# Kernel tuning notes

Hardware: AMD Instinct MI355X
Metric: run time of the kernel (lower is better)

## Reference

```python
import jax, jax.numpy as jnp
import numpy as np

NUM_HEADS = 16
NUM_KV_HEADS = 8
HEAD_DIM = 128
SCALE = 1.0 / np.sqrt(HEAD_DIM)  # 0.08838834764831845
SEQ_LENS = [1536, 512, 1024, 1024]  # ragged packed sequences, total T=4096


def setup_inputs() -> dict:
    key = jax.random.key(0)
    k1, k2, k3 = jax.random.split(key, 3)
    T = sum(SEQ_LENS)
    q = jax.random.normal(k1, (T, NUM_HEADS * HEAD_DIM), dtype=jnp.float32)
    k = jax.random.normal(k2, (T, NUM_KV_HEADS * HEAD_DIM), dtype=jnp.float32)
    v = jax.random.normal(k3, (T, NUM_KV_HEADS * HEAD_DIM), dtype=jnp.float32)
    # positions restart at 0 for each packed sequence; jumps mark boundaries
    positions = jnp.asarray(np.concatenate([np.arange(L) for L in SEQ_LENS]), dtype=jnp.int32)
    return {"q": q, "k": k, "v": v, "positions": positions}


def reference(q, k, v, positions):
    T = q.shape[0]
    G = NUM_HEADS // NUM_KV_HEADS  # GQA group size
    qh = q.reshape(T, NUM_KV_HEADS, G, HEAD_DIM)
    kh = k.reshape(T, NUM_KV_HEADS, HEAD_DIM)
    vh = v.reshape(T, NUM_KV_HEADS, HEAD_DIM)
    # segment ids from position jumps (positions[i] != positions[i-1] + 1)
    jump = jnp.concatenate([
        jnp.zeros((1,), jnp.int32),
        (positions[1:] != positions[:-1] + 1).astype(jnp.int32),
    ])
    seg = jnp.cumsum(jump)  # [T]
    idx = jnp.arange(T)
    # attend only within the same packed sequence, causally
    mask = (seg[:, None] == seg[None, :]) & (idx[:, None] >= idx[None, :])  # [T, T]
    # scores: [kv_head, group, T_q, T_k]
    scores = jnp.einsum('tkgd,skd->kgts', qh, kh) * jnp.float32(SCALE)
    scores = jnp.where(mask[None, None], scores, jnp.float32(-1e30))
    p = jax.nn.softmax(scores, axis=-1)
    o = jnp.einsum('kgts,skd->tkgd', p, vh)
    return o.reshape(T, NUM_HEADS * HEAD_DIM)
```

## Files before the change

kernel.cpp:

```cpp
#include <hip/hip_runtime.h>
#include <cstdint>
#include <cstddef>

#define NUM_KV   8
#define GQA      2
#define HD       128
#define QSTRIDE  2048
#define KSTRIDE  1024
#define SCALE_LOG2E 0.12751741032075463f

typedef float    f32x4  __attribute__((ext_vector_type(4)));
typedef float    f32x2  __attribute__((ext_vector_type(2)));
typedef float    f32x16 __attribute__((ext_vector_type(16)));
typedef unsigned u32x4  __attribute__((ext_vector_type(4)));
typedef __bf16   bf16x8 __attribute__((ext_vector_type(8)));
typedef __bf16   bf16x2 __attribute__((ext_vector_type(2)));

union U8 { unsigned short u[8]; unsigned d[4]; u32x4 q; bf16x8 v; };

__device__ __forceinline__ unsigned short f2b(float f) {
    union { float f; unsigned u; } x;
    x.f = f;
    unsigned r = x.u + 0x7fffu + ((x.u >> 16) & 1u);
    return (unsigned short)(r >> 16);
}
__device__ __forceinline__ unsigned pkb(float x, float y) {
    f32x2 f = {x, y};
    bf16x2 b = __builtin_convertvector(f, bf16x2);
    union { bf16x2 b; unsigned u; } c; c.b = b;
    return c.u;
}

#define PS_STRIDE 40

__global__ __launch_bounds__(512)
void swizzle_k(const float* __restrict__ kg, unsigned short* __restrict__ Kswz,
               int T, int NT)
{
    const int tt = blockIdx.x, h = blockIdx.y;
    const int tid = threadIdx.x;
    const int c = tid >> 6, lane = tid & 63;
    const int col = lane & 31, hk = lane >> 5;
    const int row = min(tt * 32 + col, T - 1);
    const float* src = kg + (size_t)row * KSTRIDE + h * HD + c * 16 + hk * 8;
    f32x4 a = ((const f32x4*)src)[0];
    f32x4 b = ((const f32x4*)src)[1];
    u32x4 W;
    W[0] = pkb(a[0], a[1]); W[1] = pkb(a[2], a[3]);
    W[2] = pkb(b[0], b[1]); W[3] = pkb(b[2], b[3]);
    *(u32x4*)(Kswz + (((size_t)h * NT + tt) * 8 + c) * 512 + lane * 8) = W;
}

__global__ __launch_bounds__(512)
void swizzle_v(const float* __restrict__ vg, unsigned short* __restrict__ Vswz,
               int T, int NT)
{
    const int tt = blockIdx.x, h = blockIdx.y;
    const int tid = threadIdx.x;
    const int f = tid >> 6, lane = tid & 63;
    const int col = lane & 31, hk = lane >> 5;
    const int d  = (f >> 1) * 32 + col;
    const int r0 = tt * 32 + (f & 1) * 16 + hk * 8;
    float x[8];
#pragma unroll
    for (int j = 0; j < 8; ++j) {
        const int row = min(r0 + j, T - 1);
        x[j] = vg[(size_t)row * KSTRIDE + h * HD + d];
    }
    u32x4 W;
    W[0] = pkb(x[0], x[1]); W[1] = pkb(x[2], x[3]);
    W[2] = pkb(x[4], x[5]); W[3] = pkb(x[6], x[7]);
    *(u32x4*)(Vswz + (((size_t)h * NT + tt) * 8 + f) * 512 + lane * 8) = W;
}

__global__ __launch_bounds__(256, 2)
void attn_kernel(const float* __restrict__ qg, const unsigned short* __restrict__ Kswz,
                 const unsigned short* __restrict__ Vswz, const int* __restrict__ pos,
                 float* __restrict__ out, int T, int NT)
{
    __shared__ __align__(16) float Obuf[4][32 * 128];
    __shared__ float Lb[4][32];
    __shared__ __align__(16) unsigned short Ps[4][32 * PS_STRIDE];

    const int tid  = threadIdx.x;
    const int w    = tid >> 6;
    const int lane = tid & 63;
    const int col  = lane & 31;
    const int hk   = lane >> 5;

    const int bid = blockIdx.x;
    const int kvh = bid & 7;
    const int g   = (bid >> 3) & 1;
    const int qtr = bid >> 4;
    const int nq  = (T + 31) >> 5;
    const int qt  = nq - 1 - qtr;
    const int row0 = qt * 32;
    if (row0 >= T) return;
    const int hq = kvh * GQA + g;

    const int kend = min(row0 + 32, T);
    const int k_lo = row0 - pos[row0];

    const int rbase = row0 + 4 * hk;
    int rstart[16];
#pragma unroll
    for (int r = 0; r < 16; ++r) {
        const int rg = rbase + (r & 3) + 8 * (r >> 2);
        const int rc = min(rg, T - 1);
        rstart[r] = rc - pos[rc];
    }
    int rs_max = rstart[0];
#pragma unroll
    for (int r = 1; r < 16; ++r) rs_max = max(rs_max, rstart[r]);
    rs_max = max(rs_max, __shfl_xor(rs_max, 32));

    bf16x8 qf[8];
    {
        const int qr = min(row0 + col, T - 1);
        const float* qp = qg + (size_t)qr * QSTRIDE + hq * HD + hk * 8;
#pragma unroll
        for (int c = 0; c < 8; ++c) {
            f32x4 f0 = ((const f32x4*)(qp + c * 16))[0];
            f32x4 f1 = ((const f32x4*)(qp + c * 16))[1];
            U8 u;
            u.d[0] = pkb(f0[0] * SCALE_LOG2E, f0[1] * SCALE_LOG2E);
            u.d[1] = pkb(f0[2] * SCALE_LOG2E, f0[3] * SCALE_LOG2E);
            u.d[2] = pkb(f1[0] * SCALE_LOG2E, f1[1] * SCALE_LOG2E);
            u.d[3] = pkb(f1[2] * SCALE_LOG2E, f1[3] * SCALE_LOG2E);
            qf[c] = u.v;
        }
    }

    f32x16 acc[4];
#pragma unroll
    for (int nt = 0; nt < 4; ++nt)
#pragma unroll
        for (int r = 0; r < 16; ++r) acc[nt][r] = 0.f;
    float l_vec[16];
#pragma unroll
    for (int r = 0; r < 16; ++r) l_vec[r] = 0.f;

    const int t_lo = k_lo >> 5;
    const int t_hi = (kend + 31) >> 5;
    const unsigned short* kb_base = Kswz + (size_t)kvh * NT * 4096;
    const unsigned short* vb_base = Vswz + (size_t)kvh * NT * 4096;

    U8 kf[8], kfn[8], vf[8];
    int tt = t_lo + w;
    if (tt < t_hi) {
        const unsigned short* kp = kb_base + (size_t)tt * 4096 + lane * 8;
#pragma unroll
        for (int c = 0; c < 8; ++c) kf[c].q = *(const u32x4*)(kp + c * 512);
    }

    for (; tt < t_hi; tt += 4) {
        const int ttn = tt + 4;
        if (ttn < t_hi) {
            const unsigned short* kp = kb_base + (size_t)ttn * 4096 + lane * 8;
#pragma unroll
            for (int c = 0; c < 8; ++c) kfn[c].q = *(const u32x4*)(kp + c * 512);
        }
        {
            const unsigned short* vp = vb_base + (size_t)tt * 4096 + lane * 8;
#pragma unroll
            for (int f = 0; f < 8; ++f) vf[f].q = *(const u32x4*)(vp + f * 512);
        }

        f32x16 s;
#pragma unroll
        for (int r = 0; r < 16; ++r) s[r] = 0.f;
#pragma unroll
        for (int c = 0; c < 8; ++c)
            s = __builtin_amdgcn_mfma_f32_32x32x16_bf16(qf[c], kf[c].v, s, 0, 0, 0);

        const int kb  = tt * 32;
        const int key = kb + col;
        float p[16];
        if (kb >= rs_max && kb + 32 <= row0 + 1) {
#pragma unroll
            for (int r = 0; r < 16; ++r) { p[r] = exp2f(s[r]); l_vec[r] += p[r]; }
        } else {
#pragma unroll
            for (int r = 0; r < 16; ++r) {
                const int rg = rbase + (r & 3) + 8 * (r >> 2);
                const float x = (key >= rstart[r] && key <= rg) ? s[r] : -3e38f;
                p[r] = exp2f(x);
                l_vec[r] += p[r];
            }
        }

        unsigned short* Pw = (unsigned short*)Ps[w];
#pragma unroll
        for (int r = 0; r < 16; ++r)
            Pw[((r & 3) + 8 * (r >> 2) + 4 * hk) * PS_STRIDE + col] = f2b(p[r]);
        U8 pa0, pa1;
        pa0.q = *(const u32x4*)&Pw[col * PS_STRIDE + hk * 8];
        pa1.q = *(const u32x4*)&Pw[col * PS_STRIDE + 16 + hk * 8];

#pragma unroll
        for (int nt = 0; nt < 4; ++nt) {
            acc[nt] = __builtin_amdgcn_mfma_f32_32x32x16_bf16(pa0.v, vf[nt * 2].v,     acc[nt], 0, 0, 0);
            acc[nt] = __builtin_amdgcn_mfma_f32_32x32x16_bf16(pa1.v, vf[nt * 2 + 1].v, acc[nt], 0, 0, 0);
        }
#pragma unroll
        for (int c = 0; c < 8; ++c) kf[c] = kfn[c];
    }

#pragma unroll
    for (int r = 0; r < 16; ++r) {
        float sl = l_vec[r];
        sl += __shfl_xor(sl, 1);
        sl += __shfl_xor(sl, 2);
        sl += __shfl_xor(sl, 4);
        sl += __shfl_xor(sl, 8);
        sl += __shfl_xor(sl, 16);
        if (col == 0) Lb[w][(r & 3) + 8 * (r >> 2) + 4 * hk] = sl;
    }
#pragma unroll
    for (int nt = 0; nt < 4; ++nt)
#pragma unroll
        for (int r = 0; r < 16; ++r)
            Obuf[w][((r & 3) + 8 * (r >> 2) + 4 * hk) * 128 + nt * 32 + col] = acc[nt][r];

    __syncthreads();

    const int orow = tid >> 3;
    const int oc   = (tid & 7) * 16;
    const int rg   = row0 + orow;
    const float lsum = Lb[0][orow] + Lb[1][orow] + Lb[2][orow] + Lb[3][orow];
    const float inv  = (lsum > 0.f) ? (1.0f / lsum) : 0.f;
    if (rg < T) {
        float* op = out + (size_t)rg * QSTRIDE + hq * HD + oc;
#pragma unroll
        for (int j = 0; j < 4; ++j) {
            f32x4 sv = *(const f32x4*)&Obuf[0][orow * 128 + oc + j * 4];
#pragma unroll
            for (int ww = 1; ww < 4; ++ww) {
                f32x4 t = *(const f32x4*)&Obuf[ww][orow * 128 + oc + j * 4];
                sv[0] += t[0]; sv[1] += t[1]; sv[2] += t[2]; sv[3] += t[3];
            }
            sv[0] *= inv; sv[1] *= inv; sv[2] *= inv; sv[3] *= inv;
            *(f32x4*)(op + j * 4) = sv;
        }
    }
}

extern "C" void kernel_launch(void* const* d_in, const int* in_sizes, int n_in,
                              void* d_out, int out_size, void* d_ws, size_t ws_size,
                              hipStream_t stream) {
    const float* q   = (const float*)d_in[0];
    const float* k   = (const float*)d_in[1];
    const float* v   = (const float*)d_in[2];
    const int*   pos = (const int*)d_in[3];
    float* out = (float*)d_out;
    const int T  = in_sizes[0] / QSTRIDE;
    const int NT = (T + 31) / 32;

    unsigned short* Kswz = (unsigned short*)d_ws;
    unsigned short* Vswz = Kswz + (size_t)NUM_KV * NT * 4096;

    swizzle_k<<<dim3(NT, NUM_KV), 512, 0, stream>>>(k, Kswz, T, NT);
    swizzle_v<<<dim3(NT, NUM_KV), 512, 0, stream>>>(v, Vswz, T, NT);

    attn_kernel<<<dim3(NT * 16), 256, 0, stream>>>(q, Kswz, Vswz, pos, out, T, NT);
}
```

Measured before the change: 168.9 us.

## Stage K/V swizzle through LDS and prefetch V tiles one iteration ahead

The K and V swizzle kernels now load full contiguous rows with wide vector reads into shared memory and then write the MFMA-swizzled layout from LDS. This replaces the scattered per-element strided V reads. The attention loop now double-buffers V fragments alongside K, prefetching the next tile's V so its load latency overlaps the current tile's compute. This costs more registers (an extra 8 vector fragments per lane), which could lower occupancy under the launch bound of 2 blocks.

Result: slower. 213.3 us (+26.3%).

```diff
diff --git a/kernel.cpp b/kernel.cpp
--- a/kernel.cpp
+++ b/kernel.cpp
@@ -32,45 +32,80 @@
 }
 
 #define PS_STRIDE 40
-
-__global__ __launch_bounds__(512)
+#define KL_STRIDE 136
+#define VL_STRIDE 56
+
+__global__ __launch_bounds__(256)
 void swizzle_k(const float* __restrict__ kg, unsigned short* __restrict__ Kswz,
                int T, int NT)
 {
+    __shared__ __align__(16) unsigned short Ls[32 * KL_STRIDE];
     const int tt = blockIdx.x, h = blockIdx.y;
     const int tid = threadIdx.x;
-    const int c = tid >> 6, lane = tid & 63;
+
+    {
+        const int row = tid >> 3;
+        const int d0  = (tid & 7) * 16;
+        const int rg  = min(tt * 32 + row, T - 1);
+        const float* src = kg + (size_t)rg * KSTRIDE + h * HD + d0;
+        f32x4 a = ((const f32x4*)src)[0];
+        f32x4 b = ((const f32x4*)src)[1];
+        f32x4 c = ((const f32x4*)src)[2];
+        f32x4 d = ((const f32x4*)src)[3];
+        u32x4 W0, W1;
+        W0[0] = pkb(a[0], a[1]); W0[1] = pkb(a[2], a[3]);
+        W0[2] = pkb(b[0], b[1]); W0[3] = pkb(b[2], b[3]);
+        W1[0] = pkb(c[0], c[1]); W1[1] = pkb(c[2], c[3]);
+        W1[2] = pkb(d[0], d[1]); W1[3] = pkb(d[2], d[3]);
+        *(u32x4*)&Ls[row * KL_STRIDE + d0]     = W0;
+        *(u32x4*)&Ls[row * KL_STRIDE + d0 + 8] = W1;
+    }
+    __syncthreads();
+    const int f = tid >> 6, lane = tid & 63;
     const int col = lane & 31, hk = lane >> 5;
-    const int row = min(tt * 32 + col, T - 1);
-    const float* src = kg + (size_t)row * KSTRIDE + h * HD + c * 16 + hk * 8;
-    f32x4 a = ((const f32x4*)src)[0];
-    f32x4 b = ((const f32x4*)src)[1];
-    u32x4 W;
-    W[0] = pkb(a[0], a[1]); W[1] = pkb(a[2], a[3]);
-    W[2] = pkb(b[0], b[1]); W[3] = pkb(b[2], b[3]);
-    *(u32x4*)(Kswz + (((size_t)h * NT + tt) * 8 + c) * 512 + lane * 8) = W;
-}
-
-__global__ __launch_bounds__(512)
+    unsigned short* dst = Kswz + ((size_t)h * NT + tt) * 4096 + lane * 8;
+#pragma unroll
+    for (int i = 0; i < 2; ++i) {
+        const int c = f + i * 4;
+        u32x4 W = *(const u32x4*)&Ls[col * KL_STRIDE + c * 16 + hk * 8];
+        *(u32x4*)(dst + c * 512) = W;
+    }
+}
+
+__global__ __launch_bounds__(256)
 void swizzle_v(const float* __restrict__ vg, unsigned short* __restrict__ Vswz,
                int T, int NT)
 {
+    __shared__ __align__(16) unsigned short Lsv[HD * VL_STRIDE];
     const int tt = blockIdx.x, h = blockIdx.y;
     const int tid = threadIdx.x;
+
+    {
+        const int row = tid >> 3;
+        const int d0  = (tid & 7) * 16;
+        const int rg  = min(tt * 32 + row, T - 1);
+        const float* src = vg + (size_t)rg * KSTRIDE + h * HD + d0;
+        f32x4 x[4];
+#pragma unroll
+        for (int j = 0; j < 4; ++j) x[j] = ((const f32x4*)src)[j];
+#pragma unroll
+        for (int j = 0; j < 4; ++j)
+#pragma unroll
+            for (int e = 0; e < 4; ++e)
+                Lsv[(d0 + j * 4 + e) * VL_STRIDE + row] = f2b(x[j][e]);
+    }
+    __syncthreads();
     const int f = tid >> 6, lane = tid & 63;
     const int col = lane & 31, hk = lane >> 5;
-    const int d  = (f >> 1) * 32 + col;
-    const int r0 = tt * 32 + (f & 1) * 16 + hk * 8;
-    float x[8];
-#pragma unroll
-    for (int j = 0; j < 8; ++j) {
-        const int row = min(r0 + j, T - 1);
-        x[j] = vg[(size_t)row * KSTRIDE + h * HD + d];
-    }
-    u32x4 W;
-    W[0] = pkb(x[0], x[1]); W[1] = pkb(x[2], x[3]);
-    W[2] = pkb(x[4], x[5]); W[3] = pkb(x[6], x[7]);
-    *(u32x4*)(Vswz + (((size_t)h * NT + tt) * 8 + f) * 512 + lane * 8) = W;
+    unsigned short* dst = Vswz + ((size_t)h * NT + tt) * 4096 + lane * 8;
+#pragma unroll
+    for (int i = 0; i < 2; ++i) {
+        const int ff = f + i * 4;
+        const int d    = (ff >> 1) * 32 + col;
+        const int key0 = (ff & 1) * 16 + hk * 8;
+        u32x4 W = *(const u32x4*)&Lsv[d * VL_STRIDE + key0];
+        *(u32x4*)(dst + ff * 512) = W;
+    }
 }
 
 __global__ __launch_bounds__(256, 2)
@@ -142,28 +177,29 @@
 
     const int t_lo = k_lo >> 5;
     const int t_hi = (kend + 31) >> 5;
-    const unsigned short* kb_base = Kswz + (size_t)kvh * NT * 4096;
-    const unsigned short* vb_base = Vswz + (size_t)kvh * NT * 4096;
-
-    U8 kf[8], kfn[8], vf[8];
+    const unsigned short* kb_base = Kswz + (size_t)kvh * NT * 4096 + lane * 8;
+    const unsigned short* vb_base = Vswz + (size_t)kvh * NT * 4096 + lane * 8;
+
+    U8 kf[8], kfn[8], vf[8], vfn[8];
     int tt = t_lo + w;
     if (tt < t_hi) {
-        const unsigned short* kp = kb_base + (size_t)tt * 4096 + lane * 8;
+        const unsigned short* kp = kb_base + (size_t)tt * 4096;
+        const unsigned short* vp = vb_base + (size_t)tt * 4096;
 #pragma unroll
         for (int c = 0; c < 8; ++c) kf[c].q = *(const u32x4*)(kp + c * 512);
+#pragma unroll
+        for (int c = 0; c < 8; ++c) vf[c].q = *(const u32x4*)(vp + c * 512);
     }
 
     for (; tt < t_hi; tt += 4) {
         const int ttn = tt + 4;
         if (ttn < t_hi) {
-            const unsigned short* kp = kb_base + (size_t)ttn * 4096 + lane * 8;
+            const unsigned short* kp = kb_base + (size_t)ttn * 4096;
+            const unsigned short* vp = vb_base + (size_t)ttn * 4096;
 #pragma unroll
             for (int c = 0; c < 8; ++c) kfn[c].q = *(const u32x4*)(kp + c * 512);
-        }
-        {
-            const unsigned short* vp = vb_base + (size_t)tt * 4096 + lane * 8;
-#pragma unroll
-            for (int f = 0; f < 8; ++f) vf[f].q = *(const u32x4*)(vp + f * 512);
+#pragma unroll
+            for (int c = 0; c < 8; ++c) vfn[c].q = *(const u32x4*)(vp + c * 512);
         }
 
         f32x16 s;
@@ -203,7 +239,7 @@
             acc[nt] = __builtin_amdgcn_mfma_f32_32x32x16_bf16(pa1.v, vf[nt * 2 + 1].v, acc[nt], 0, 0, 0);
         }
 #pragma unroll
-        for (int c = 0; c < 8; ++c) kf[c] = kfn[c];
+        for (int c = 0; c < 8; ++c) { kf[c] = kfn[c]; vf[c] = vfn[c]; }
     }
 
 #pragma unroll
@@ -259,8 +295,8 @@
     unsigned short* Kswz = (unsigned short*)d_ws;
     unsigned short* Vswz = Kswz + (size_t)NUM_KV * NT * 4096;
 
-    swizzle_k<<<dim3(NT, NUM_KV), 512, 0, stream>>>(k, Kswz, T, NT);
-    swizzle_v<<<dim3(NT, NUM_KV), 512, 0, stream>>>(v, Vswz, T, NT);
+    swizzle_k<<<dim3(NT, NUM_KV), 256, 0, stream>>>(k, Kswz, T, NT);
+    swizzle_v<<<dim3(NT, NUM_KV), 256, 0, stream>>>(v, Vswz, T, NT);
 
     attn_kernel<<<dim3(NT * 16), 256, 0, stream>>>(q, Kswz, Vswz, pos, out, T, NT);
 }
```
